# Performance work log

Measured on AMD Instinct MI355X. Metric: run time of the kernel, lower is better.

The kernel has to match this reference:

```python
import jax, jax.numpy as jnp
import numpy as np

D_MODEL = 1024
N_HEADS = 16
D_K = D_MODEL // N_HEADS


def setup_inputs() -> dict:
    key = jax.random.key(0)
    ks = jax.random.split(key, 7)
    B, S, D = 2, 2048, D_MODEL
    scale = 1.0 / np.sqrt(D)
    return {
        "query": jax.random.normal(ks[0], (B, S, D), dtype=jnp.float32),
        "key": jax.random.normal(ks[1], (B, S, D), dtype=jnp.float32),
        "value": jax.random.normal(ks[2], (B, S, D), dtype=jnp.float32),
        "w_q": jax.random.normal(ks[3], (D, D), dtype=jnp.float32) * scale,
        "w_k": jax.random.normal(ks[4], (D, D), dtype=jnp.float32) * scale,
        "w_v": jax.random.normal(ks[5], (D, D), dtype=jnp.float32) * scale,
        "w_o": jax.random.normal(ks[6], (D, D), dtype=jnp.float32) * scale,
    }


def reference(query, key, value, w_q, w_k, w_v, w_o):
    B, S, D = query.shape
    H, Dk = N_HEADS, D_K
    # nn.Linear (no bias): x @ W.T ; then split heads -> [B, H, S, Dk]
    def split_heads(x, W):
        return (x @ W.T).reshape(B, S, H, Dk).transpose(0, 2, 1, 3)
    Q = split_heads(query, w_q)
    K = split_heads(key, w_k)
    V = split_heads(value, w_v)
    scores = jnp.einsum("bhqd,bhkd->bhqk", Q, K) / np.sqrt(Dk).astype(jnp.float32)
    attn = jax.nn.softmax(scores, axis=-1)  # dropout is identity in eval
    attended = jnp.einsum("bhqk,bhkd->bhqd", attn, V)
    attended = attended.transpose(0, 2, 1, 3).reshape(B, S, D)
    output = attended @ w_o.T
    avg_attention = attn.mean(axis=1)  # mean over heads -> [B, S, S]
    return (output, avg_attention)
```

## Files before the change

kernel.cpp:

```cpp
#include <hip/hip_runtime.h>
#include <math.h>

#define SEQ 2048
#define DMODEL 1024
#define NH 16
#define DK 64
#define BATCH 2

using bf16x8 = __attribute__((ext_vector_type(8))) __bf16;
using bf16x4 = __attribute__((ext_vector_type(4))) __bf16;
using f32x4  = __attribute__((ext_vector_type(4))) float;

__device__ inline f32x4 mfma16(bf16x8 a, bf16x8 b, f32x4 c) {
    return __builtin_amdgcn_mfma_f32_16x16x32_bf16(a, b, c, 0, 0, 0);
}

__device__ inline void load_lds16(const void* g, void* l) {
    __builtin_amdgcn_global_load_lds(
        (const __attribute__((address_space(1))) void*)g,
        (__attribute__((address_space(3))) void*)l, 16, 0, 0);
}

#define VMCNT(n) asm volatile("s_waitcnt vmcnt(" #n ")" ::: "memory")
#define BARRIER() __builtin_amdgcn_s_barrier()
#define CFENCE() asm volatile("" ::: "memory")
#define EXP_SCALE 0.18033688011112042f
#define EXP2(x) __builtin_amdgcn_exp2f(x)

__global__ __launch_bounds__(256) void conv_bf16(
        const float* __restrict__ q, const float* __restrict__ k,
        const float* __restrict__ v, const float* __restrict__ wq,
        const float* __restrict__ wk, const float* __restrict__ wv,
        const float* __restrict__ wo,
        __bf16* __restrict__ oq, __bf16* __restrict__ ok, __bf16* __restrict__ ov,
        __bf16* __restrict__ owq, __bf16* __restrict__ owk,
        __bf16* __restrict__ owv, __bf16* __restrict__ owo) {
    int bid = blockIdx.x;
    const float* src;
    __bf16* dst;
    size_t off;
    if (bid < 3072) {
        int ti = bid >> 10;
        src = ti == 0 ? q : (ti == 1 ? k : v);
        dst = ti == 0 ? oq : (ti == 1 ? ok : ov);
        off = (size_t)(bid & 1023) * 4096;
    } else {
        int ti = (bid - 3072) >> 8;
        src = ti == 0 ? wq : (ti == 1 ? wk : (ti == 2 ? wv : wo));
        dst = ti == 0 ? owq : (ti == 1 ? owk : (ti == 2 ? owv : owo));
        off = (size_t)((bid - 3072) & 255) * 4096;
    }
    src += off; dst += off;
    const int t = threadIdx.x;
#pragma unroll
    for (int i = 0; i < 4; ++i) {
        float4 x = *(const float4*)(src + t * 4 + i * 1024);
        bf16x4 y;
        y[0] = (__bf16)x.x; y[1] = (__bf16)x.y;
        y[2] = (__bf16)x.z; y[3] = (__bf16)x.w;
        *(bf16x4*)(dst + t * 4 + i * 1024) = y;
    }
}

__device__ __forceinline__ void gemm256_core(const __bf16* __restrict__ A,
                                             const __bf16* __restrict__ B,
                                             void* __restrict__ out, int mode,
                                             int m0, int n0, int N,
                                             __bf16* As, __bf16* Bs) {
    const int t    = threadIdx.x;
    const int w    = t >> 6;
    const int lane = t & 63;
    const int m    = lane & 15;
    const int kg   = lane >> 4;
    const int wr   = w >> 2, wc = w & 3;

    auto stage = [&](int buf, int k0) {
        const __bf16* ga = A + (size_t)(m0 + w * 16 + m) * 1024 + k0 + kg * 8;
        load_lds16(ga, &As[buf * 4096 + w * 512]);
        const __bf16* gb0 = B + (size_t)(n0 + (2 * w) * 16 + m) * 1024 + k0 + kg * 8;
        load_lds16(gb0, &Bs[buf * 8192 + (2 * w) * 512]);
        const __bf16* gb1 = B + (size_t)(n0 + (2 * w + 1) * 16 + m) * 1024 + k0 + kg * 8;
        load_lds16(gb1, &Bs[buf * 8192 + (2 * w + 1) * 512]);
    };

    f32x4 acc[4][4] = {};

    stage(0, 0);
    CFENCE();
    stage(1, 32);

    int cb = 0, sb = 2;
    for (int ts = 0; ts < 32; ++ts) {
        if (ts < 30) {
            stage(sb, (ts + 2) * 32);
            VMCNT(6);
        } else if (ts == 30) {
            VMCNT(3);
        } else {
            VMCNT(0);
        }
        BARRIER();
        CFENCE();
        const __bf16* Ac = &As[cb * 4096];
        const __bf16* Bc = &Bs[cb * 8192];
        bf16x8 af[4], bg[4];
#pragma unroll
        for (int i = 0; i < 4; ++i)
            af[i] = *(const bf16x8*)&Ac[(wr * 4 + i) * 512 + lane * 8];
#pragma unroll
        for (int j = 0; j < 4; ++j)
            bg[j] = *(const bf16x8*)&Bc[(wc * 4 + j) * 512 + lane * 8];
        __builtin_amdgcn_s_setprio(1);
#pragma unroll
        for (int i = 0; i < 4; ++i)
#pragma unroll
            for (int j = 0; j < 4; ++j)
                acc[i][j] = mfma16(af[i], bg[j], acc[i][j]);
        __builtin_amdgcn_s_setprio(0);
        BARRIER();
        cb = cb == 2 ? 0 : cb + 1;
        sb = sb == 2 ? 0 : sb + 1;
    }

#pragma unroll
    for (int i = 0; i < 4; ++i) {
        const int rb = m0 + wr * 64 + i * 16 + kg * 4;
#pragma unroll
        for (int j = 0; j < 4; ++j) {
            const int gc = n0 + wc * 64 + j * 16 + m;
#pragma unroll
            for (int r = 0; r < 4; ++r) {
                const int gr = rb + r;
                const float vv = acc[i][j][r];
                if (mode == 0) {
                    ((float*)out)[(size_t)gr * N + gc] = vv;
                } else if (mode == 1) {
                    ((__bf16*)out)[(size_t)gr * N + gc] = (__bf16)vv;
                } else {
                    const int hh = gr >> 6, dd = gr & 63;
                    const int bb = gc >> 11, ss = gc & 2047;
                    ((__bf16*)out)[(((size_t)bb * NH + hh) * DK + dd) * SEQ + ss] = (__bf16)vv;
                }
            }
        }
    }
}

__device__ __forceinline__ int xcd_swz(int s, int cpx) {
    return (s & 7) * cpx + (s >> 3);
}

__global__ __launch_bounds__(512, 4) void gemm_qkv(
        const __bf16* __restrict__ Xq, const __bf16* __restrict__ Wq, __bf16* Qr,
        const __bf16* __restrict__ Xk, const __bf16* __restrict__ Wk, __bf16* Kr,
        const __bf16* __restrict__ Xv, const __bf16* __restrict__ Wv, __bf16* Vt) {
    __shared__ __align__(16) __bf16 As[12288];
    __shared__ __align__(16) __bf16 Bs[24576];
    const int bid = blockIdx.x;
    if (bid < 128) {
        const int s = xcd_swz(bid, 16);
        gemm256_core(Xq, Wq, Qr, 1, (s >> 2) * 128, (s & 3) * 256, 1024, As, Bs);
    } else if (bid < 256) {
        const int s = xcd_swz(bid - 128, 16);
        gemm256_core(Xk, Wk, Kr, 1, (s >> 2) * 128, (s & 3) * 256, 1024, As, Bs);
    } else {
        const int s = xcd_swz(bid - 256, 16);
        gemm256_core(Wv, Xv, Vt, 2, (s >> 4) * 128, (s & 15) * 256, 4096, As, Bs);
    }
}

__global__ __launch_bounds__(512, 4) void attn_flash(const __bf16* __restrict__ Qr,
                                                     const __bf16* __restrict__ Kr,
                                                     const __bf16* __restrict__ Vt,
                                                     __bf16* __restrict__ att,
                                                     float* __restrict__ invs) {
    __shared__ __align__(16) unsigned char smem[66048];
    __bf16* Kb   = (__bf16*)smem;
    __bf16* Vb   = Kb + 16384;
    float*  sinv = (float*)(smem + 65536);

    const int t    = threadIdx.x;
    const int w    = t >> 6;
    const int lane = t & 63;
    const int m    = lane & 15;
    const int kg   = lane >> 4;

    const int L  = xcd_swz(blockIdx.x, 64);
    const int b  = L >> 8;
    const int h  = (L >> 4) & 15;
    const int qw = (L & 15) * 128 + w * 16;

    const __bf16* Kh = Kr + (size_t)b * SEQ * 1024 + h * 64;
    const __bf16* Vh = Vt + ((size_t)b * NH + h) * DK * SEQ;

    const size_t rowQ = (size_t)(b * SEQ + qw + m) * 1024 + h * 64 + kg * 8;
    const bf16x8 qa = *(const bf16x8*)(Qr + rowQ);
    const bf16x8 qb = *(const bf16x8*)(Qr + rowQ + 32);
    CFENCE();

    auto kaddr = [&](int bk, int kt) {
        const int f = bk >> 1, dh = bk & 1, i = lane & 15;
        const int key = (f >> 1) * 32 + (i >> 2) * 8 + (f & 1) * 4 + (i & 3);
        return (const void*)(Kh + (size_t)(kt + key) * 1024 + dh * 32 + (lane >> 4) * 8);
    };
    auto vaddr = [&](int bv, int kt) {
        const int nt = bv >> 2, ks = bv & 3, i = lane & 15;
        return (const void*)(Vh + (size_t)(nt * 16 + i) * SEQ + kt + ks * 32 + (lane >> 4) * 8);
    };
    auto stage = [&](int buf, int kt) {
        load_lds16(kaddr(w, kt),     Kb + buf * 8192 + w * 512);
        load_lds16(kaddr(w + 8, kt), Kb + buf * 8192 + (w + 8) * 512);
        load_lds16(vaddr(w, kt),     Vb + buf * 8192 + w * 512);
        load_lds16(vaddr(w + 8, kt), Vb + buf * 8192 + (w + 8) * 512);
    };

    f32x4 pv[4] = {};
    float rsum = 0.f;

    stage(0, 0);

    int cur = 0;
    for (int ts = 0; ts < 16; ++ts) {
        if (ts + 1 < 16) {
            stage(cur ^ 1, (ts + 1) * 128);
            VMCNT(4);
        } else {
            VMCNT(0);
        }
        BARRIER();
        CFENCE();
        const __bf16* Kc = Kb + cur * 8192;
        const __bf16* Vc = Vb + cur * 8192;
        bf16x4 pk[8];
#pragma unroll
        for (int f = 0; f < 8; ++f) {
            bf16x8 k0 = *(const bf16x8*)&Kc[(f * 2 + 0) * 512 + lane * 8];
            bf16x8 k1 = *(const bf16x8*)&Kc[(f * 2 + 1) * 512 + lane * 8];
            f32x4 c = {};
            c = mfma16(k0, qa, c);
            c = mfma16(k1, qb, c);
            bf16x4 t4;
#pragma unroll
            for (int r = 0; r < 4; ++r) {
                float pe = EXP2(c[r] * EXP_SCALE);
                rsum += pe;
                t4[r] = (__bf16)pe;
            }
            pk[f] = t4;
        }
        __builtin_amdgcn_s_setprio(1);
#pragma unroll
        for (int ks = 0; ks < 4; ++ks) {
            bf16x8 pa;
#pragma unroll
            for (int e = 0; e < 4; ++e) {
                pa[e]     = pk[2 * ks][e];
                pa[4 + e] = pk[2 * ks + 1][e];
            }
#pragma unroll
            for (int nt = 0; nt < 4; ++nt) {
                bf16x8 vb = *(const bf16x8*)&Vc[(nt * 4 + ks) * 512 + lane * 8];
                pv[nt] = mfma16(pa, vb, pv[nt]);
            }
        }
        __builtin_amdgcn_s_setprio(0);
        BARRIER();
        cur ^= 1;
    }

    rsum += __shfl_xor(rsum, 16);
    rsum += __shfl_xor(rsum, 32);
    const float inv = 1.0f / rsum;
    if (lane < 16) {
        sinv[w * 16 + m] = inv;
        invs[((size_t)b * NH + h) * SEQ + qw + m] = inv;
    }
    __syncthreads();
    float iv[4];
#pragma unroll
    for (int r = 0; r < 4; ++r) iv[r] = sinv[w * 16 + kg * 4 + r];

    float* scf = (float*)smem + w * 1088;
#pragma unroll
    for (int nt = 0; nt < 4; ++nt)
#pragma unroll
        for (int r = 0; r < 4; ++r)
            scf[(kg * 4 + r) * 68 + nt * 16 + m] = pv[nt][r] * iv[r];
    __syncthreads();
    {
        const int q = lane >> 2, c0 = (lane & 3) * 16;
        const float* srcf = &scf[q * 68 + c0];
        bf16x8 o0, o1;
#pragma unroll
        for (int j = 0; j < 8; ++j) {
            o0[j] = (__bf16)srcf[j];
            o1[j] = (__bf16)srcf[j + 8];
        }
        __bf16* dst = att + (size_t)(b * SEQ + qw + q) * DMODEL + h * DK + c0;
        *(bf16x8*)(dst)     = o0;
        *(bf16x8*)(dst + 8) = o1;
    }
}

__device__ __forceinline__ void avg8_core(const __bf16* __restrict__ Qr,
                                          const __bf16* __restrict__ Kr,
                                          const float* __restrict__ invs,
                                          float* __restrict__ avg,
                                          int L, __bf16* Kb) {
    const int t    = threadIdx.x;
    const int w    = t >> 6;
    const int lane = t & 63;
    const int m    = lane & 15;
    const int kg   = lane >> 4;
    const int b    = L >> 8;
    const int s0   = ((L >> 4) & 15) * 128;
    const int qw   = (L & 15) * 128 + w * 16;

    const __bf16* Kbase = Kr + (size_t)(b * SEQ + s0) * 1024;

    auto stageK = [&](int buf, int h) {
#pragma unroll
        for (int s = 0; s < 2; ++s) {
            const int i   = w * 2 + s;
            const int row = i * 8 + (lane >> 3);
            const int u   = lane & 7;
            load_lds16(Kbase + (size_t)row * 1024 + h * 64 + ((u ^ (row & 7)) * 8),
                       Kb + buf * 8192 + i * 512);
        }
    };

    f32x4 acc[8] = {};

    stageK(0, 0);
    const size_t qoff = (size_t)(b * SEQ + qw + m) * 1024 + kg * 8;
    bf16x8 a0 = *(const bf16x8*)(Qr + qoff);
    bf16x8 a1 = *(const bf16x8*)(Qr + qoff + 32);
    f32x4 ivr = *(const f32x4*)&invs[(size_t)b * NH * SEQ + qw + kg * 4];
    __syncthreads();

    int cur = 0;
    for (int h = 0; h < NH; ++h) {
        if (h + 1 < NH) stageK(cur ^ 1, h + 1);
        bf16x8 na0, na1;
        f32x4 nivr;
        if (h + 1 < NH) {
            na0  = *(const bf16x8*)(Qr + qoff + (h + 1) * 64);
            na1  = *(const bf16x8*)(Qr + qoff + (h + 1) * 64 + 32);
            nivr = *(const f32x4*)&invs[((size_t)b * NH + h + 1) * SEQ + qw + kg * 4];
        }
        const __bf16* Kc = Kb + cur * 8192;
#pragma unroll
        for (int nt = 0; nt < 8; ++nt) {
            const int row = nt * 16 + m;
            bf16x8 k0 = *(const bf16x8*)&Kc[row * 64 + ((kg ^ (m & 7)) * 8)];
            bf16x8 k1 = *(const bf16x8*)&Kc[row * 64 + (((kg + 4) ^ (m & 7)) * 8)];
            f32x4 c = {};
            c = mfma16(a0, k0, c);
            c = mfma16(a1, k1, c);
#pragma unroll
            for (int r = 0; r < 4; ++r)
                acc[nt][r] += ivr[r] * EXP2(c[r] * EXP_SCALE);
        }
        __syncthreads();
        cur ^= 1;
        a0 = na0; a1 = na1; ivr = nivr;
    }

    const float sc = 1.0f / NH;
#pragma unroll
    for (int nt = 0; nt < 8; ++nt)
#pragma unroll
        for (int r = 0; r < 4; ++r)
            avg[(size_t)(b * SEQ + qw + kg * 4 + r) * SEQ + s0 + nt * 16 + m] =
                acc[nt][r] * sc;
}

__global__ __launch_bounds__(512, 4) void gemm_wo_avg(
        const __bf16* __restrict__ At, const __bf16* __restrict__ Wo,
        float* __restrict__ out,
        const __bf16* __restrict__ Qr, const __bf16* __restrict__ Kr,
        const float* __restrict__ invs, float* __restrict__ avg) {
    __shared__ __align__(16) __bf16 sm[36864];
    const int bid = blockIdx.x;
    if (bid < 128) {
        const int s = xcd_swz(bid, 16);
        gemm256_core(At, Wo, out, 0, (s >> 2) * 128, (s & 3) * 256, 1024,
                     sm, sm + 12288);
    } else {
        avg8_core(Qr, Kr, invs, avg, xcd_swz(bid - 128, 64), sm);
    }
}

extern "C" void kernel_launch(void* const* d_in, const int* in_sizes, int n_in,
                              void* d_out, int out_size, void* d_ws, size_t ws_size,
                              hipStream_t stream) {
    const float* query = (const float*)d_in[0];
    const float* key   = (const float*)d_in[1];
    const float* value = (const float*)d_in[2];
    const float* w_q   = (const float*)d_in[3];
    const float* w_k   = (const float*)d_in[4];
    const float* w_v   = (const float*)d_in[5];
    const float* w_o   = (const float*)d_in[6];

    float* out = (float*)d_out;
    float* avg = out + (size_t)BATCH * SEQ * DMODEL;

    __bf16* Xq = (__bf16*)d_ws;
    __bf16* Xk = Xq + 4194304;
    __bf16* Xv = Xk + 4194304;
    __bf16* Wq = Xv + 4194304;
    __bf16* Wk = Wq + 1048576;
    __bf16* Wv = Wk + 1048576;
    __bf16* Wo = Wv + 1048576;
    __bf16* Qr = Wo + 1048576;
    __bf16* Kr = Qr + 4194304;
    __bf16* Vt = Kr + 4194304;
    float*  Invs = (float*)(Vt + 4194304);
    __bf16* At = Xq;

    conv_bf16<<<4096, 256, 0, stream>>>(query, key, value, w_q, w_k, w_v, w_o,
                                        Xq, Xk, Xv, Wq, Wk, Wv, Wo);

    gemm_qkv<<<384, 512, 0, stream>>>(Xq, Wq, Qr, Xk, Wk, Kr, Xv, Wv, Vt);

    attn_flash<<<512, 512, 0, stream>>>(Qr, Kr, Vt, At, Invs);

    gemm_wo_avg<<<640, 512, 0, stream>>>(At, Wo, out, Qr, Kr, Invs, avg);
}
```

Baseline: 249.3 us.

## Switch QKV projection GEMM to 128x128 tiles with 256 threads and 4-stage ring

Result: slower. 257.1 us (+3.1%).

```diff
diff --git a/kernel.cpp b/kernel.cpp
--- a/kernel.cpp
+++ b/kernel.cpp
@@ -62,25 +62,27 @@
     }
 }
 
-__device__ __forceinline__ void gemm256_core(const __bf16* __restrict__ A,
-                                             const __bf16* __restrict__ B,
-                                             void* __restrict__ out, int mode,
-                                             int m0, int n0, int N,
-                                             __bf16* As, __bf16* Bs) {
+__device__ __forceinline__ void gemm_core(const __bf16* __restrict__ A,
+                                          const __bf16* __restrict__ B,
+                                          void* __restrict__ out, int mode,
+                                          int m0, int n0, int N,
+                                          __bf16* As, __bf16* Bs) {
     const int t    = threadIdx.x;
     const int w    = t >> 6;
     const int lane = t & 63;
     const int m    = lane & 15;
     const int kg   = lane >> 4;
-    const int wr   = w >> 2, wc = w & 3;
+    const int wr   = w >> 1, wc = w & 1;
 
     auto stage = [&](int buf, int k0) {
-        const __bf16* ga = A + (size_t)(m0 + w * 16 + m) * 1024 + k0 + kg * 8;
-        load_lds16(ga, &As[buf * 4096 + w * 512]);
-        const __bf16* gb0 = B + (size_t)(n0 + (2 * w) * 16 + m) * 1024 + k0 + kg * 8;
-        load_lds16(gb0, &Bs[buf * 8192 + (2 * w) * 512]);
-        const __bf16* gb1 = B + (size_t)(n0 + (2 * w + 1) * 16 + m) * 1024 + k0 + kg * 8;
-        load_lds16(gb1, &Bs[buf * 8192 + (2 * w + 1) * 512]);
+        const __bf16* ga0 = A + (size_t)(m0 + w * 16 + m) * 1024 + k0 + kg * 8;
+        load_lds16(ga0, &As[buf * 4096 + w * 512]);
+        const __bf16* ga1 = A + (size_t)(m0 + (w + 4) * 16 + m) * 1024 + k0 + kg * 8;
+        load_lds16(ga1, &As[buf * 4096 + (w + 4) * 512]);
+        const __bf16* gb0 = B + (size_t)(n0 + w * 16 + m) * 1024 + k0 + kg * 8;
+        load_lds16(gb0, &Bs[buf * 4096 + w * 512]);
+        const __bf16* gb1 = B + (size_t)(n0 + (w + 4) * 16 + m) * 1024 + k0 + kg * 8;
+        load_lds16(gb1, &Bs[buf * 4096 + (w + 4) * 512]);
     };
 
     f32x4 acc[4][4] = {};
@@ -89,20 +91,19 @@
     CFENCE();
     stage(1, 32);
 
-    int cb = 0, sb = 2;
     for (int ts = 0; ts < 32; ++ts) {
-        if (ts < 30) {
-            stage(sb, (ts + 2) * 32);
-            VMCNT(6);
-        } else if (ts == 30) {
-            VMCNT(3);
+        if (ts + 2 < 32) {
+            stage((ts + 2) & 3, (ts + 2) * 32);
+            VMCNT(8);
+        } else if (ts + 1 < 32) {
+            VMCNT(4);
         } else {
             VMCNT(0);
         }
         BARRIER();
         CFENCE();
-        const __bf16* Ac = &As[cb * 4096];
-        const __bf16* Bc = &Bs[cb * 8192];
+        const __bf16* Ac = &As[(ts & 3) * 4096];
+        const __bf16* Bc = &Bs[(ts & 3) * 4096];
         bf16x8 af[4], bg[4];
 #pragma unroll
         for (int i = 0; i < 4; ++i)
@@ -117,9 +118,6 @@
             for (int j = 0; j < 4; ++j)
                 acc[i][j] = mfma16(af[i], bg[j], acc[i][j]);
         __builtin_amdgcn_s_setprio(0);
-        BARRIER();
-        cb = cb == 2 ? 0 : cb + 1;
-        sb = sb == 2 ? 0 : sb + 1;
     }
 
 #pragma unroll
@@ -146,26 +144,110 @@
     }
 }
 
+__device__ __forceinline__ void gemm256_core(const __bf16* __restrict__ A,
+                                             const __bf16* __restrict__ B,
+                                             void* __restrict__ out, int mode,
+                                             int m0, int n0, int N,
+                                             __bf16* As, __bf16* Bs) {
+    const int t    = threadIdx.x;
+    const int w    = t >> 6;
+    const int lane = t & 63;
+    const int m    = lane & 15;
+    const int kg   = lane >> 4;
+    const int wr   = w >> 2, wc = w & 3;
+
+    auto stage = [&](int buf, int k0) {
+        const __bf16* ga = A + (size_t)(m0 + w * 16 + m) * 1024 + k0 + kg * 8;
+        load_lds16(ga, &As[buf * 4096 + w * 512]);
+        const __bf16* gb0 = B + (size_t)(n0 + (2 * w) * 16 + m) * 1024 + k0 + kg * 8;
+        load_lds16(gb0, &Bs[buf * 8192 + (2 * w) * 512]);
+        const __bf16* gb1 = B + (size_t)(n0 + (2 * w + 1) * 16 + m) * 1024 + k0 + kg * 8;
+        load_lds16(gb1, &Bs[buf * 8192 + (2 * w + 1) * 512]);
+    };
+
+    f32x4 acc[4][4] = {};
+
+    stage(0, 0);
+    CFENCE();
+    stage(1, 32);
+
+    int cb = 0, sb = 2;
+    for (int ts = 0; ts < 32; ++ts) {
+        if (ts < 30) {
+            stage(sb, (ts + 2) * 32);
+            VMCNT(6);
+        } else if (ts == 30) {
+            VMCNT(3);
+        } else {
+            VMCNT(0);
+        }
+        BARRIER();
+        CFENCE();
+        const __bf16* Ac = &As[cb * 4096];
+        const __bf16* Bc = &Bs[cb * 8192];
+        bf16x8 af[4], bg[4];
+#pragma unroll
+        for (int i = 0; i < 4; ++i)
+            af[i] = *(const bf16x8*)&Ac[(wr * 4 + i) * 512 + lane * 8];
+#pragma unroll
+        for (int j = 0; j < 4; ++j)
+            bg[j] = *(const bf16x8*)&Bc[(wc * 4 + j) * 512 + lane * 8];
+        __builtin_amdgcn_s_setprio(1);
+#pragma unroll
+        for (int i = 0; i < 4; ++i)
+#pragma unroll
+            for (int j = 0; j < 4; ++j)
+                acc[i][j] = mfma16(af[i], bg[j], acc[i][j]);
+        __builtin_amdgcn_s_setprio(0);
+        BARRIER();
+        cb = cb == 2 ? 0 : cb + 1;
+        sb = sb == 2 ? 0 : sb + 1;
+    }
+
+#pragma unroll
+    for (int i = 0; i < 4; ++i) {
+        const int rb = m0 + wr * 64 + i * 16 + kg * 4;
+#pragma unroll
+        for (int j = 0; j < 4; ++j) {
+            const int gc = n0 + wc * 64 + j * 16 + m;
+#pragma unroll
+            for (int r = 0; r < 4; ++r) {
+                const int gr = rb + r;
+                const float vv = acc[i][j][r];
+                if (mode == 0) {
+                    ((float*)out)[(size_t)gr * N + gc] = vv;
+                } else if (mode == 1) {
+                    ((__bf16*)out)[(size_t)gr * N + gc] = (__bf16)vv;
+                } else {
+                    const int hh = gr >> 6, dd = gr & 63;
+                    const int bb = gc >> 11, ss = gc & 2047;
+                    ((__bf16*)out)[(((size_t)bb * NH + hh) * DK + dd) * SEQ + ss] = (__bf16)vv;
+                }
+            }
+        }
+    }
+}
+
 __device__ __forceinline__ int xcd_swz(int s, int cpx) {
     return (s & 7) * cpx + (s >> 3);
 }
 
-__global__ __launch_bounds__(512, 4) void gemm_qkv(
+__global__ __launch_bounds__(256, 2) void gemm_qkv(
         const __bf16* __restrict__ Xq, const __bf16* __restrict__ Wq, __bf16* Qr,
         const __bf16* __restrict__ Xk, const __bf16* __restrict__ Wk, __bf16* Kr,
         const __bf16* __restrict__ Xv, const __bf16* __restrict__ Wv, __bf16* Vt) {
-    __shared__ __align__(16) __bf16 As[12288];
-    __shared__ __align__(16) __bf16 Bs[24576];
+    __shared__ __align__(16) __bf16 As[16384];
+    __shared__ __align__(16) __bf16 Bs[16384];
     const int bid = blockIdx.x;
-    if (bid < 128) {
-        const int s = xcd_swz(bid, 16);
-        gemm256_core(Xq, Wq, Qr, 1, (s >> 2) * 128, (s & 3) * 256, 1024, As, Bs);
-    } else if (bid < 256) {
-        const int s = xcd_swz(bid - 128, 16);
-        gemm256_core(Xk, Wk, Kr, 1, (s >> 2) * 128, (s & 3) * 256, 1024, As, Bs);
+    if (bid < 256) {
+        const int s = xcd_swz(bid, 32);
+        gemm_core(Xq, Wq, Qr, 1, (s >> 3) * 128, (s & 7) * 128, 1024, As, Bs);
+    } else if (bid < 512) {
+        const int s = xcd_swz(bid - 256, 32);
+        gemm_core(Xk, Wk, Kr, 1, (s >> 3) * 128, (s & 7) * 128, 1024, As, Bs);
     } else {
-        const int s = xcd_swz(bid - 256, 16);
-        gemm256_core(Wv, Xv, Vt, 2, (s >> 4) * 128, (s & 15) * 256, 4096, As, Bs);
+        const int s = xcd_swz(bid - 512, 32);
+        gemm_core(Wv, Xv, Vt, 2, (s >> 5) * 128, (s & 31) * 128, 4096, As, Bs);
     }
 }
 
@@ -421,7 +503,7 @@
     conv_bf16<<<4096, 256, 0, stream>>>(query, key, value, w_q, w_k, w_v, w_o,
                                         Xq, Xk, Xv, Wq, Wk, Wv, Wo);
 
-    gemm_qkv<<<384, 512, 0, stream>>>(Xq, Wq, Qr, Xk, Wk, Kr, Xv, Wv, Vt);
+    gemm_qkv<<<768, 256, 0, stream>>>(Xq, Wq, Qr, Xk, Wk, Kr, Xv, Wv, Vt);
 
     attn_flash<<<512, 512, 0, stream>>>(Qr, Kr, Vt, At, Invs);
 
```

## Process two query tiles per wave in flash attention, halving block size

Applied to the files above, without the earlier changes.

Result: no change. 253.6 us (+1.7%).

```diff
diff --git a/kernel.cpp b/kernel.cpp
--- a/kernel.cpp
+++ b/kernel.cpp
@@ -169,7 +169,7 @@
     }
 }
 
-__global__ __launch_bounds__(512, 4) void attn_flash(const __bf16* __restrict__ Qr,
+__global__ __launch_bounds__(256, 2) void attn_flash(const __bf16* __restrict__ Qr,
                                                      const __bf16* __restrict__ Kr,
                                                      const __bf16* __restrict__ Vt,
                                                      __bf16* __restrict__ att,
@@ -193,9 +193,12 @@
     const __bf16* Kh = Kr + (size_t)b * SEQ * 1024 + h * 64;
     const __bf16* Vh = Vt + ((size_t)b * NH + h) * DK * SEQ;
 
-    const size_t rowQ = (size_t)(b * SEQ + qw + m) * 1024 + h * 64 + kg * 8;
-    const bf16x8 qa = *(const bf16x8*)(Qr + rowQ);
-    const bf16x8 qb = *(const bf16x8*)(Qr + rowQ + 32);
+    const size_t rowQ0 = (size_t)(b * SEQ + qw + m) * 1024 + h * 64 + kg * 8;
+    const size_t rowQ1 = rowQ0 + (size_t)64 * 1024;
+    const bf16x8 qa0 = *(const bf16x8*)(Qr + rowQ0);
+    const bf16x8 qb0 = *(const bf16x8*)(Qr + rowQ0 + 32);
+    const bf16x8 qa1 = *(const bf16x8*)(Qr + rowQ1);
+    const bf16x8 qb1 = *(const bf16x8*)(Qr + rowQ1 + 32);
     CFENCE();
 
     auto kaddr = [&](int bk, int kt) {
@@ -208,14 +211,16 @@
         return (const void*)(Vh + (size_t)(nt * 16 + i) * SEQ + kt + ks * 32 + (lane >> 4) * 8);
     };
     auto stage = [&](int buf, int kt) {
-        load_lds16(kaddr(w, kt),     Kb + buf * 8192 + w * 512);
-        load_lds16(kaddr(w + 8, kt), Kb + buf * 8192 + (w + 8) * 512);
-        load_lds16(vaddr(w, kt),     Vb + buf * 8192 + w * 512);
-        load_lds16(vaddr(w + 8, kt), Vb + buf * 8192 + (w + 8) * 512);
+#pragma unroll
+        for (int s = 0; s < 4; ++s) {
+            const int bk = w + s * 4;
+            load_lds16(kaddr(bk, kt), Kb + buf * 8192 + bk * 512);
+            load_lds16(vaddr(bk, kt), Vb + buf * 8192 + bk * 512);
+        }
     };
 
-    f32x4 pv[4] = {};
-    float rsum = 0.f;
+    f32x4 pv0[4] = {}, pv1[4] = {};
+    float rsum0 = 0.f, rsum1 = 0.f;
 
     stage(0, 0);
 
@@ -223,7 +228,7 @@
     for (int ts = 0; ts < 16; ++ts) {
         if (ts + 1 < 16) {
             stage(cur ^ 1, (ts + 1) * 128);
-            VMCNT(4);
+            VMCNT(8);
         } else {
             VMCNT(0);
         }
@@ -231,36 +236,46 @@
         CFENCE();
         const __bf16* Kc = Kb + cur * 8192;
         const __bf16* Vc = Vb + cur * 8192;
-        bf16x4 pk[8];
+        bf16x4 pk0[8], pk1[8];
 #pragma unroll
         for (int f = 0; f < 8; ++f) {
             bf16x8 k0 = *(const bf16x8*)&Kc[(f * 2 + 0) * 512 + lane * 8];
             bf16x8 k1 = *(const bf16x8*)&Kc[(f * 2 + 1) * 512 + lane * 8];
-            f32x4 c = {};
-            c = mfma16(k0, qa, c);
-            c = mfma16(k1, qb, c);
-            bf16x4 t4;
+            f32x4 c0 = {};
+            c0 = mfma16(k0, qa0, c0);
+            c0 = mfma16(k1, qb0, c0);
+            f32x4 c1 = {};
+            c1 = mfma16(k0, qa1, c1);
+            c1 = mfma16(k1, qb1, c1);
+            bf16x4 t0, t1;
 #pragma unroll
             for (int r = 0; r < 4; ++r) {
-                float pe = EXP2(c[r] * EXP_SCALE);
-                rsum += pe;
-                t4[r] = (__bf16)pe;
+                float p0 = EXP2(c0[r] * EXP_SCALE);
+                rsum0 += p0;
+                t0[r] = (__bf16)p0;
+                float p1 = EXP2(c1[r] * EXP_SCALE);
+                rsum1 += p1;
+                t1[r] = (__bf16)p1;
             }
-            pk[f] = t4;
+            pk0[f] = t0;
+            pk1[f] = t1;
         }
         __builtin_amdgcn_s_setprio(1);
 #pragma unroll
         for (int ks = 0; ks < 4; ++ks) {
-            bf16x8 pa;
+            bf16x8 pa0, pa1;
 #pragma unroll
             for (int e = 0; e < 4; ++e) {
-                pa[e]     = pk[2 * ks][e];
-                pa[4 + e] = pk[2 * ks + 1][e];
+                pa0[e]     = pk0[2 * ks][e];
+                pa0[4 + e] = pk0[2 * ks + 1][e];
+                pa1[e]     = pk1[2 * ks][e];
+                pa1[4 + e] = pk1[2 * ks + 1][e];
             }
 #pragma unroll
             for (int nt = 0; nt < 4; ++nt) {
                 bf16x8 vb = *(const bf16x8*)&Vc[(nt * 4 + ks) * 512 + lane * 8];
-                pv[nt] = mfma16(pa, vb, pv[nt]);
+                pv0[nt] = mfma16(pa0, vb, pv0[nt]);
+                pv1[nt] = mfma16(pa1, vb, pv1[nt]);
             }
         }
         __builtin_amdgcn_s_setprio(0);
@@ -268,37 +283,54 @@
         cur ^= 1;
     }
 
-    rsum += __shfl_xor(rsum, 16);
-    rsum += __shfl_xor(rsum, 32);
-    const float inv = 1.0f / rsum;
+    rsum0 += __shfl_xor(rsum0, 16);
+    rsum0 += __shfl_xor(rsum0, 32);
+    rsum1 += __shfl_xor(rsum1, 16);
+    rsum1 += __shfl_xor(rsum1, 32);
+    const float inv0 = 1.0f / rsum0;
+    const float inv1 = 1.0f / rsum1;
     if (lane < 16) {
-        sinv[w * 16 + m] = inv;
-        invs[((size_t)b * NH + h) * SEQ + qw + m] = inv;
+        sinv[(w * 2 + 0) * 16 + m] = inv0;
+        sinv[(w * 2 + 1) * 16 + m] = inv1;
+        invs[((size_t)b * NH + h) * SEQ + qw + m]      = inv0;
+        invs[((size_t)b * NH + h) * SEQ + qw + 64 + m] = inv1;
     }
     __syncthreads();
-    float iv[4];
-#pragma unroll
-    for (int r = 0; r < 4; ++r) iv[r] = sinv[w * 16 + kg * 4 + r];
-
-    float* scf = (float*)smem + w * 1088;
+    float iv0[4], iv1[4];
+#pragma unroll
+    for (int r = 0; r < 4; ++r) {
+        iv0[r] = sinv[(w * 2 + 0) * 16 + kg * 4 + r];
+        iv1[r] = sinv[(w * 2 + 1) * 16 + kg * 4 + r];
+    }
+
+    float* s0 = (float*)smem + (w * 2 + 0) * 1088;
+    float* s1 = (float*)smem + (w * 2 + 1) * 1088;
 #pragma unroll
     for (int nt = 0; nt < 4; ++nt)
 #pragma unroll
-        for (int r = 0; r < 4; ++r)
-            scf[(kg * 4 + r) * 68 + nt * 16 + m] = pv[nt][r] * iv[r];
+        for (int r = 0; r < 4; ++r) {
+            s0[(kg * 4 + r) * 68 + nt * 16 + m] = pv0[nt][r] * iv0[r];
+            s1[(kg * 4 + r) * 68 + nt * 16 + m] = pv1[nt][r] * iv1[r];
+        }
     __syncthreads();
     {
         const int q = lane >> 2, c0 = (lane & 3) * 16;
-        const float* srcf = &scf[q * 68 + c0];
-        bf16x8 o0, o1;
+        const float* src0 = &s0[q * 68 + c0];
+        const float* src1 = &s1[q * 68 + c0];
+        bf16x8 o0, o1, o2, o3;
 #pragma unroll
         for (int j = 0; j < 8; ++j) {
-            o0[j] = (__bf16)srcf[j];
-            o1[j] = (__bf16)srcf[j + 8];
-        }
-        __bf16* dst = att + (size_t)(b * SEQ + qw + q) * DMODEL + h * DK + c0;
-        *(bf16x8*)(dst)     = o0;
-        *(bf16x8*)(dst + 8) = o1;
+            o0[j] = (__bf16)src0[j];
+            o1[j] = (__bf16)src0[j + 8];
+            o2[j] = (__bf16)src1[j];
+            o3[j] = (__bf16)src1[j + 8];
+        }
+        __bf16* d0 = att + (size_t)(b * SEQ + qw + q) * DMODEL + h * DK + c0;
+        __bf16* d1 = att + (size_t)(b * SEQ + qw + 64 + q) * DMODEL + h * DK + c0;
+        *(bf16x8*)(d0)     = o0;
+        *(bf16x8*)(d0 + 8) = o1;
+        *(bf16x8*)(d1)     = o2;
+        *(bf16x8*)(d1 + 8) = o3;
     }
 }
 
@@ -423,7 +455,7 @@
 
     gemm_qkv<<<384, 512, 0, stream>>>(Xq, Wq, Qr, Xk, Wk, Kr, Xv, Wv, Vt);
 
-    attn_flash<<<512, 512, 0, stream>>>(Qr, Kr, Vt, At, Invs);
+    attn_flash<<<512, 256, 0, stream>>>(Qr, Kr, Vt, At, Invs);
 
     gemm_wo_avg<<<640, 512, 0, stream>>>(At, Wo, out, Qr, Kr, Invs, avg);
 }
```
